# Kernel optimization log

Measured on AMD Instinct MI355X. Metric: run time of the kernel, lower is better.

Reference implementation:

```python
import jax, jax.numpy as jnp
import numpy as np
from jax import lax

DT = 0.1

def setup_inputs() -> dict:
    key = jax.random.key(0)
    ks = jax.random.split(key, 6)
    T, B, D, H, O = 4096, 16, 256, 256, 256
    x = jax.random.normal(ks[0], (T, B, D), dtype=jnp.float32)
    U_w = jax.random.normal(ks[1], (H, D), dtype=jnp.float32) / np.sqrt(D)
    U_b = jax.random.normal(ks[2], (H,), dtype=jnp.float32) * 0.1
    # underlying parameter of the ExpLambda parametrization: weight = expm(W_log)
    W_log = jax.random.normal(ks[3], (H, H), dtype=jnp.float32) * 0.01
    c_w = jax.random.normal(ks[4], (O, H), dtype=jnp.float32) / np.sqrt(H)
    c_b = jax.random.normal(ks[5], (O,), dtype=jnp.float32) * 0.1
    return {"x": x, "U_w": U_w, "U_b": U_b, "W_log": W_log, "c_w": c_w, "c_b": c_b}

def reference(x, U_w, U_b, W_log, c_w, c_b):
    # x: [T, B, D] (time-major, matching torch.transpose(x,0,1) in the original)
    T, B, D = x.shape
    H = W_log.shape[0]
    Wexp = jax.scipy.linalg.expm(W_log)          # parametrized recurrent weight
    u = jnp.einsum('tbd,hd->tbh', x, U_w) + U_b  # precompute U(x) for all steps

    def step(h, u_t):
        # h_next = h + dt * tanh(u_t - W h)
        h_next = h + DT * jnp.tanh(u_t - h @ Wexp.T)
        return h_next, h_next

    h0 = jnp.zeros((B, H), dtype=x.dtype)
    h_final, hidden = lax.scan(step, h0, u)       # hidden: [T, B, H]
    out = jnp.einsum('tbh,oh->tbo', hidden, c_w) + c_b
    # original returns h_next.unsqueeze(1) on a (1,B,H) tensor -> (1,1,B,H)
    return out, h_final[None, None]
```

## Files before the change

### kernel.cpp

```cpp
#include <hip/hip_runtime.h>
#include <math.h>

#define T_STEPS 4096
#define NB 16
#define NH 256
#define BH (NB * NH)
#define DT_STEP 0.1f

typedef __attribute__((ext_vector_type(8))) short short8;
typedef __attribute__((ext_vector_type(4))) float f32x4;

__global__ __launch_bounds__(1024) void k_init_S(const float* __restrict__ A,
                                                 float* __restrict__ S) {
    int idx = blockIdx.x * 1024 + threadIdx.x;
    int i = idx >> 8, j = idx & 255;
    S[idx] = A[idx] + (i == j ? 1.0f : 0.0f);
}

__global__ __launch_bounds__(256) void k_expm_term(const float* __restrict__ Pprev,
                                                   const float* __restrict__ A,
                                                   float* __restrict__ Pnew,
                                                   float* __restrict__ S,
                                                   float invk) {
    __shared__ float prow[256];
    int i = blockIdx.x, j = threadIdx.x;
    prow[j] = Pprev[i * 256 + j];
    __syncthreads();
    float acc = 0.f;
#pragma unroll 8
    for (int m = 0; m < 256; ++m) acc = fmaf(prow[m], A[m * 256 + j], acc);
    float v = acc * invk;
    Pnew[i * 256 + j] = v;
    S[i * 256 + j] += v;
}

__global__ __launch_bounds__(256) void k_gemm_rows(const float* __restrict__ X,
                                                   const float* __restrict__ Wm,
                                                   const float* __restrict__ bias,
                                                   float* __restrict__ Out) {
    __shared__ float4 xs4[16][64];
    const int tid = threadIdx.x;
    const long r0 = (long)blockIdx.x * 16;
    float* xs = (float*)xs4;
#pragma unroll
    for (int rr = 0; rr < 16; ++rr) xs[rr * 256 + tid] = X[(r0 + rr) * 256 + tid];
    __syncthreads();

    float acc[16];
#pragma unroll
    for (int rr = 0; rr < 16; ++rr) acc[rr] = 0.f;

    const float4* wrow = (const float4*)(Wm + tid * 256);
    for (int d4 = 0; d4 < 64; ++d4) {
        float4 w = wrow[d4];
#pragma unroll
        for (int rr = 0; rr < 16; ++rr) {
            float4 xv = xs4[rr][d4];
            acc[rr] = fmaf(w.x, xv.x, acc[rr]);
            acc[rr] = fmaf(w.y, xv.y, acc[rr]);
            acc[rr] = fmaf(w.z, xv.z, acc[rr]);
            acc[rr] = fmaf(w.w, xv.w, acc[rr]);
        }
    }
    float b = bias[tid];
#pragma unroll
    for (int rr = 0; rr < 16; ++rr) Out[(r0 + rr) * 256 + tid] = acc[rr] + b;
}

__global__ __launch_bounds__(1024, 4)
void k_scan_mfma(const float* __restrict__ u,
                 const float* __restrict__ S,
                 float* __restrict__ hidden,
                 float* __restrict__ hfin) {
    const int b   = blockIdx.x;
    const int tid = threadIdx.x;
    const int w   = tid >> 6;
    const int l   = tid & 63;
    const int n   = (w << 4) | (l & 15);
    const int kg  = l >> 4;

    __shared__ uint4 lds4[1152];
    char* lds = (char*)lds4;
    for (int i = tid; i < 1152; i += 1024) lds4[i] = uint4{0, 0, 0, 0};

    union Frag { unsigned int u[4]; short8 v; };
    Frag ef[8];
#pragma unroll
    for (int kt = 0; kt < 8; ++kt) {
        const int k0 = kt * 32 + kg * 8;
        const float* sp = S + (size_t)n * 256 + k0;
        float e[8];
#pragma unroll
        for (int j = 0; j < 8; ++j)
            e[j] = sp[j] - ((n == k0 + j) ? 1.0f : 0.0f);
#pragma unroll
        for (int r2 = 0; r2 < 4; ++r2) {
            unsigned int pk;
            asm volatile("v_cvt_pk_bf16_f32 %0, %1, %2"
                         : "=v"(pk) : "v"(e[2 * r2]), "v"(e[2 * r2 + 1]));
            ef[kt].u[r2] = pk;
        }
    }

    Frag af[8];
#pragma unroll
    for (int kt = 0; kt < 8; ++kt) {
        af[kt].u[0] = 0; af[kt].u[1] = 0; af[kt].u[2] = 0; af[kt].u[3] = 0;
    }
    const bool areal = ((l & 15) == 0);
    const int  abase = l * 16 + kg * 32;

    const bool wr  = (l < 16);
    const int  col = (w << 4) | l;
    const int  wg  = (col >> 3) & 3;
    const int  wby = (col >> 5) * 1152 + wg * 288 + ((col & 7) >> 1) * 4;

    const float* up = u + (size_t)b * NH + col;
    float* hp = hidden + (size_t)b * NH + col;

    float hval = 0.f, u_cur = 0.f, u_nxt = 0.f;
    if (wr) {
        u_cur = up[0];
        u_nxt = up[BH];
    }
    __syncthreads();

    int roff = 0;
    for (int t = 0; t < T_STEPS; ++t) {
        float u_n2 = 0.f;
        if (wr && t + 2 < T_STEPS) u_n2 = up[(size_t)(t + 2) * BH];

        if (areal) {
#pragma unroll
            for (int kt = 0; kt < 8; ++kt)
                af[kt].v = *(const short8*)(lds + roff + kt * 1152 + abase);
        }

        f32x4 acc = {0.f, 0.f, 0.f, 0.f};
#pragma unroll
        for (int kt = 0; kt < 8; ++kt)
            acc = __builtin_amdgcn_mfma_f32_16x16x32_bf16(af[kt].v, ef[kt].v, acc, 0, 0, 0);

        if (wr) {
            float y  = acc[0];
            float xa = (u_cur - hval) - y;
            float E2 = __expf(2.0f * xa);
            float th = fmaf(-2.0f, __builtin_amdgcn_rcpf(E2 + 1.0f), 1.0f);
            hval = fmaf(DT_STEP, th, hval);
            hp[(size_t)t * BH] = hval;
            int nb = __builtin_amdgcn_mov_dpp(__float_as_int(hval), 0xB1, 0xF, 0xF, true);
            if ((l & 1) == 0) {
                unsigned int pk;
                asm volatile("v_cvt_pk_bf16_f32 %0, %1, %2"
                             : "=v"(pk) : "v"(hval), "v"(__int_as_float(nb)));
                *(unsigned int*)(lds + (roff ^ 9216) + wby) = pk;
            }
        }
        u_cur = u_nxt;
        u_nxt = u_n2;
        roff ^= 9216;
        __syncthreads();
    }
    if (wr) hfin[(size_t)b * NH + col] = hval;
}

extern "C" void kernel_launch(void* const* d_in, const int* in_sizes, int n_in,
                              void* d_out, int out_size, void* d_ws, size_t ws_size,
                              hipStream_t stream) {
    const float* x     = (const float*)d_in[0];
    const float* U_w   = (const float*)d_in[1];
    const float* U_b   = (const float*)d_in[2];
    const float* W_log = (const float*)d_in[3];
    const float* c_w   = (const float*)d_in[4];
    const float* c_b   = (const float*)d_in[5];

    float* out    = (float*)d_out;
    float* hidden = out;
    float* hfin   = out + (long)T_STEPS * BH;

    float* ws = (float*)d_ws;
    float* S  = ws;
    float* Pa = ws + 65536;
    float* Pb = ws + 2 * 65536;
    float* u  = ws + 3 * 65536;

    k_init_S<<<64, 1024, 0, stream>>>(W_log, S);
    const float* prev = W_log;
    float* cur = Pa;
    for (int k = 2; k <= 9; ++k) {
        k_expm_term<<<256, 256, 0, stream>>>(prev, W_log, cur, S, 1.0f / (float)k);
        prev = cur;
        cur = (cur == Pa) ? Pb : Pa;
    }

    k_gemm_rows<<<4096, 256, 0, stream>>>(x, U_w, U_b, u);

    k_scan_mfma<<<NB, 1024, 0, stream>>>(u, S, hidden, hfin);

    k_gemm_rows<<<4096, 256, 0, stream>>>(hidden, c_w, c_b, hidden);
}
```

Baseline: 2.335 ms.

## Restructure recurrent scan to 4 waves with broadcast h operand and full-lane MFMA use

The per-batch recurrence kernel now runs with 256 threads (4 waves) instead of 1024. Each wave holds four 16-row tiles of the bf16 recurrent weight in registers and issues four MFMA chains that share one broadcast h fragment read from a small 1 KB double-buffered LDS vector. All 64 lanes now own one hidden unit each, instead of only 16 lanes per wave doing useful work. The aim is to make the per-step barrier cheaper and cut the LDS traffic and idle lanes on the serial critical path. In exchange each wave runs four times as many MFMAs per step and holds more registers.

```diff
diff --git a/kernel.cpp b/kernel.cpp
--- a/kernel.cpp
+++ b/kernel.cpp
@@ -67,101 +67,107 @@
     for (int rr = 0; rr < 16; ++rr) Out[(r0 + rr) * 256 + tid] = acc[rr] + b;
 }
 
-__global__ __launch_bounds__(1024, 4)
-void k_scan_mfma(const float* __restrict__ u,
-                 const float* __restrict__ S,
-                 float* __restrict__ hidden,
-                 float* __restrict__ hfin) {
+__global__ __launch_bounds__(256)
+__attribute__((amdgpu_waves_per_eu(1, 1)))
+void k_scan_bc(const float* __restrict__ u,
+               const float* S,
+               float* hidden,
+               float* __restrict__ hfin) {
     const int b   = blockIdx.x;
     const int tid = threadIdx.x;
     const int w   = tid >> 6;
     const int l   = tid & 63;
-    const int n   = (w << 4) | (l & 15);
-    const int kg  = l >> 4;
-
-    __shared__ uint4 lds4[1152];
-    char* lds = (char*)lds4;
-    for (int i = tid; i < 1152; i += 1024) lds4[i] = uint4{0, 0, 0, 0};
+    const int lg  = l >> 4;
+    const int lr  = l & 15;
+
+    __shared__ unsigned int hlds[256];
+    char* lds = (char*)hlds;
 
     union Frag { unsigned int u[4]; short8 v; };
-    Frag ef[8];
-#pragma unroll
-    for (int kt = 0; kt < 8; ++kt) {
-        const int k0 = kt * 32 + kg * 8;
-        const float* sp = S + (size_t)n * 256 + k0;
-        float e[8];
-#pragma unroll
-        for (int j = 0; j < 8; ++j)
-            e[j] = sp[j] - ((n == k0 + j) ? 1.0f : 0.0f);
-#pragma unroll
-        for (int r2 = 0; r2 < 4; ++r2) {
+
+    Frag ef[4][8];
+#pragma unroll
+    for (int j = 0; j < 4; ++j) {
+        const int n = ((4 * w + j) << 4) | lr;
+#pragma unroll
+        for (int kt = 0; kt < 8; ++kt) {
+            const int k0 = kt * 32 + lg * 8;
+            const float* sp = S + (size_t)n * 256 + k0;
+            float e[8];
+#pragma unroll
+            for (int q = 0; q < 8; ++q)
+                e[q] = sp[q] - ((n == k0 + q) ? 1.0f : 0.0f);
+#pragma unroll
+            for (int r2 = 0; r2 < 4; ++r2) {
+                unsigned int pk;
+                asm volatile("v_cvt_pk_bf16_f32 %0, %1, %2"
+                             : "=v"(pk) : "v"(e[2 * r2]), "v"(e[2 * r2 + 1]));
+                ef[j][kt].u[r2] = pk;
+            }
+        }
+    }
+
+    const int j_own = (l >> 2) & 3;
+    const int n_own = (w << 6) | (j_own << 4) | (lg << 2) | (l & 3);
+
+    if (tid < 256) hlds[tid] = 0u;
+
+    const float* up = u + (size_t)b * NH + n_own;
+    float* hp = hidden + (size_t)b * NH + n_own;
+
+    float hval = 0.f;
+    float u_cur = up[0];
+    float u_nxt = up[BH];
+    __syncthreads();
+
+    int roff = 0;
+    for (int t = 0; t < T_STEPS; ++t) {
+        const int tpre = (t + 2 < T_STEPS) ? (t + 2) : (T_STEPS - 1);
+        float u_n2 = up[(size_t)tpre * BH];
+
+        Frag hb[8];
+#pragma unroll
+        for (int kt = 0; kt < 8; ++kt)
+            hb[kt].v = *(const short8*)(lds + roff + kt * 64 + lg * 16);
+
+        f32x4 ac0 = {0.f, 0.f, 0.f, 0.f};
+        f32x4 ac1 = {0.f, 0.f, 0.f, 0.f};
+        f32x4 ac2 = {0.f, 0.f, 0.f, 0.f};
+        f32x4 ac3 = {0.f, 0.f, 0.f, 0.f};
+#pragma unroll
+        for (int kt = 0; kt < 8; ++kt) {
+            ac0 = __builtin_amdgcn_mfma_f32_16x16x32_bf16(ef[0][kt].v, hb[kt].v, ac0, 0, 0, 0);
+            ac1 = __builtin_amdgcn_mfma_f32_16x16x32_bf16(ef[1][kt].v, hb[kt].v, ac1, 0, 0, 0);
+            ac2 = __builtin_amdgcn_mfma_f32_16x16x32_bf16(ef[2][kt].v, hb[kt].v, ac2, 0, 0, 0);
+            ac3 = __builtin_amdgcn_mfma_f32_16x16x32_bf16(ef[3][kt].v, hb[kt].v, ac3, 0, 0, 0);
+        }
+
+        f32x4 ca = (j_own & 1) ? ac1 : ac0;
+        f32x4 cb = (j_own & 1) ? ac3 : ac2;
+        f32x4 cc = (j_own & 2) ? cb : ca;
+        float y01 = (l & 1) ? cc[1] : cc[0];
+        float y23 = (l & 1) ? cc[3] : cc[2];
+        float y   = (l & 2) ? y23 : y01;
+
+        float xa = (u_cur - hval) - y;
+        float E2 = __expf(2.0f * xa);
+        float th = fmaf(-2.0f, __builtin_amdgcn_rcpf(E2 + 1.0f), 1.0f);
+        hval = fmaf(DT_STEP, th, hval);
+        hp[(size_t)t * BH] = hval;
+
+        int nb = __builtin_amdgcn_mov_dpp(__float_as_int(hval), 0xB1, 0xF, 0xF, true);
+        if ((l & 1) == 0) {
             unsigned int pk;
             asm volatile("v_cvt_pk_bf16_f32 %0, %1, %2"
-                         : "=v"(pk) : "v"(e[2 * r2]), "v"(e[2 * r2 + 1]));
-            ef[kt].u[r2] = pk;
-        }
-    }
-
-    Frag af[8];
-#pragma unroll
-    for (int kt = 0; kt < 8; ++kt) {
-        af[kt].u[0] = 0; af[kt].u[1] = 0; af[kt].u[2] = 0; af[kt].u[3] = 0;
-    }
-    const bool areal = ((l & 15) == 0);
-    const int  abase = l * 16 + kg * 32;
-
-    const bool wr  = (l < 16);
-    const int  col = (w << 4) | l;
-    const int  wg  = (col >> 3) & 3;
-    const int  wby = (col >> 5) * 1152 + wg * 288 + ((col & 7) >> 1) * 4;
-
-    const float* up = u + (size_t)b * NH + col;
-    float* hp = hidden + (size_t)b * NH + col;
-
-    float hval = 0.f, u_cur = 0.f, u_nxt = 0.f;
-    if (wr) {
-        u_cur = up[0];
-        u_nxt = up[BH];
-    }
-    __syncthreads();
-
-    int roff = 0;
-    for (int t = 0; t < T_STEPS; ++t) {
-        float u_n2 = 0.f;
-        if (wr && t + 2 < T_STEPS) u_n2 = up[(size_t)(t + 2) * BH];
-
-        if (areal) {
-#pragma unroll
-            for (int kt = 0; kt < 8; ++kt)
-                af[kt].v = *(const short8*)(lds + roff + kt * 1152 + abase);
-        }
-
-        f32x4 acc = {0.f, 0.f, 0.f, 0.f};
-#pragma unroll
-        for (int kt = 0; kt < 8; ++kt)
-            acc = __builtin_amdgcn_mfma_f32_16x16x32_bf16(af[kt].v, ef[kt].v, acc, 0, 0, 0);
-
-        if (wr) {
-            float y  = acc[0];
-            float xa = (u_cur - hval) - y;
-            float E2 = __expf(2.0f * xa);
-            float th = fmaf(-2.0f, __builtin_amdgcn_rcpf(E2 + 1.0f), 1.0f);
-            hval = fmaf(DT_STEP, th, hval);
-            hp[(size_t)t * BH] = hval;
-            int nb = __builtin_amdgcn_mov_dpp(__float_as_int(hval), 0xB1, 0xF, 0xF, true);
-            if ((l & 1) == 0) {
-                unsigned int pk;
-                asm volatile("v_cvt_pk_bf16_f32 %0, %1, %2"
-                             : "=v"(pk) : "v"(hval), "v"(__int_as_float(nb)));
-                *(unsigned int*)(lds + (roff ^ 9216) + wby) = pk;
-            }
+                         : "=v"(pk) : "v"(hval), "v"(__int_as_float(nb)));
+            *(unsigned int*)(lds + (roff ^ 512) + ((n_own >> 1) << 2)) = pk;
         }
         u_cur = u_nxt;
         u_nxt = u_n2;
-        roff ^= 9216;
+        roff ^= 512;
         __syncthreads();
     }
-    if (wr) hfin[(size_t)b * NH + col] = hval;
+    hfin[(size_t)b * NH + n_own] = hval;
 }
 
 extern "C" void kernel_launch(void* const* d_in, const int* in_sizes, int n_in,
@@ -195,7 +201,7 @@
 
     k_gemm_rows<<<4096, 256, 0, stream>>>(x, U_w, U_b, u);
 
-    k_scan_mfma<<<NB, 1024, 0, stream>>>(u, S, hidden, hfin);
+    k_scan_bc<<<NB, 256, 0, stream>>>(u, S, hidden, hfin);
 
     k_gemm_rows<<<4096, 256, 0, stream>>>(hidden, c_w, c_b, hidden);
 }
```

Measured after the change: 2.491 ms. 6.7% more time.
